# Optimization experiments

Hardware: AMD Instinct MI355X
Metric: run time of the kernel (lower is better)

Reference implementation:

```python
import jax, jax.numpy as jnp
import numpy as np

H = W = 240

def setup_inputs() -> dict:
    key = jax.random.key(0)
    k1, k2, k3 = jax.random.split(key, 3)
    B = 256
    T2_Gen = jax.random.normal(k1, (B, 1, H, W), dtype=jnp.float32)
    underT2_K = jax.random.normal(k2, (B, 2, H, W), dtype=jnp.float32)
    # k-space sampling mask (soft in [0,1); original uses a fixed undersampling mask)
    A = jax.random.uniform(k3, (H, W), dtype=jnp.float32)
    return {"T2_Gen": T2_Gen, "underT2_K": underT2_K, "A": A}

def reference(T2_Gen, underT2_K, A):
    # x2: [B, H, W]
    x2 = T2_Gen.reshape(-1, H, W)
    # batched 2D FFT over the last two axes (replaces the per-slice numpy loop)
    x2_k = jnp.fft.fft2(x2)  # complex64
    # undersampled k-space as complex: real = channel 0, imag = channel 1
    y_k = underT2_K[:, 0, :, :] + 1j * underT2_K[:, 1, :, :]
    z_k = (1.0 - A) * x2_k + y_k
    z = jnp.abs(jnp.fft.ifft2(z_k))  # [B, H, W] real
    return z.reshape(-1, 1, H, W)
```

## Files before the change

kernel.cpp:

```cpp
#include <hip/hip_runtime.h>
#include <hip/hip_fp16.h>
#include <math.h>

#define HW 240
#define PITCH 241
#define IMG_PIX (HW*HW)
#define NB 15
#define TILE_ELEMS (240*16)

__device__ __forceinline__ float2 cmul(float2 a, float2 b){
    return make_float2(a.x*b.x - a.y*b.y, a.x*b.y + a.y*b.x);
}
__device__ __forceinline__ float2 cadd(float2 a, float2 b){
    return make_float2(a.x+b.x, a.y+b.y);
}
__device__ __forceinline__ float2 csub(float2 a, float2 b){
    return make_float2(a.x-b.x, a.y-b.y);
}
__device__ __forceinline__ __half2 f2h(float2 a){ return __floats2half2_rn(a.x, a.y); }
__device__ __forceinline__ float2 h2f(__half2 h){ return make_float2(__low2float(h), __high2float(h)); }

template<int SIGN>
__device__ __forceinline__ void dft15(const float2* x, float2* X){
    const float S = (float)SIGN;
    const float s3 = 0.8660254037844387f;
    float2 y[5][3];
    #pragma unroll
    for (int n2 = 0; n2 < 5; ++n2){
        float2 a0 = x[n2], a1 = x[5+n2], a2 = x[10+n2];
        float2 t = cadd(a1, a2);
        float2 u = csub(a1, a2);
        float2 m = make_float2(a0.x - 0.5f*t.x, a0.y - 0.5f*t.y);
        float sx = S * s3;
        float2 s = make_float2(-sx*u.y, sx*u.x);
        y[n2][0] = cadd(a0, t);
        y[n2][1] = cadd(m, s);
        y[n2][2] = csub(m, s);
    }
    const float C15[9] = {1.f, 0.9135454576426009f, 0.6691306063588582f, 0.30901699437494745f,
                          -0.10452846326765346f, -0.5f, -0.8090169943749475f,
                          -0.9781476007338057f, -0.9781476007338057f};
    const float S15[9] = {0.f, 0.4067366430758004f, 0.7431448254773942f, 0.9510565162951535f,
                          0.9945218953682733f, 0.8660254037844387f, 0.5877852522924731f,
                          0.20791169081775931f, -0.20791169081775931f};
    #pragma unroll
    for (int n2 = 1; n2 < 5; ++n2){
        #pragma unroll
        for (int k1 = 1; k1 < 3; ++k1){
            const int e = n2*k1;
            y[n2][k1] = cmul(y[n2][k1], make_float2(C15[e], S*S15[e]));
        }
    }
    const float c1 = 0.30901699437494745f, s1 = 0.9510565162951535f;
    const float c2 = -0.8090169943749475f, s2 = 0.5877852522924731f;
    #pragma unroll
    for (int k1 = 0; k1 < 3; ++k1){
        float2 x0 = y[0][k1], x1 = y[1][k1], x2 = y[2][k1], x3 = y[3][k1], x4 = y[4][k1];
        float2 t1 = cadd(x1, x4), t3 = csub(x1, x4);
        float2 t2 = cadd(x2, x3), t4 = csub(x2, x3);
        X[k1] = make_float2(x0.x + t1.x + t2.x, x0.y + t1.y + t2.y);
        float2 u1 = make_float2(x0.x + c1*t1.x + c2*t2.x, x0.y + c1*t1.y + c2*t2.y);
        float2 u2 = make_float2(x0.x + c2*t1.x + c1*t2.x, x0.y + c2*t1.y + c1*t2.y);
        float2 v1 = make_float2(S*(s1*t3.x + s2*t4.x), S*(s1*t3.y + s2*t4.y));
        float2 v2 = make_float2(S*(s2*t3.x - s1*t4.x), S*(s2*t3.y - s1*t4.y));
        X[k1+3]  = make_float2(u1.x - v1.y, u1.y + v1.x);
        X[k1+12] = make_float2(u1.x + v1.y, u1.y - v1.x);
        X[k1+6]  = make_float2(u2.x - v2.y, u2.y + v2.x);
        X[k1+9]  = make_float2(u2.x + v2.y, u2.y - v2.x);
    }
}

template<int SIGN>
__device__ __forceinline__ void dft16(const float2* x, float2* X){
    const float S = (float)SIGN;
    float2 y[4][4];
    #pragma unroll
    for (int n2 = 0; n2 < 4; ++n2){
        float2 a0 = x[n2], a1 = x[4+n2], a2 = x[8+n2], a3 = x[12+n2];
        float2 t0 = cadd(a0,a2), t1 = csub(a0,a2);
        float2 t2 = cadd(a1,a3), t3 = csub(a1,a3);
        float2 it3 = make_float2(-S*t3.y, S*t3.x);
        y[n2][0] = cadd(t0,t2);
        y[n2][2] = csub(t0,t2);
        y[n2][1] = cadd(t1,it3);
        y[n2][3] = csub(t1,it3);
    }
    const float C16[10] = {1.f, 0.9238795325112867f, 0.7071067811865476f, 0.3826834323650898f,
                           0.f, -0.3826834323650898f, -0.7071067811865476f, -0.9238795325112867f,
                           -1.f, -0.9238795325112867f};
    const float S16[10] = {0.f, 0.3826834323650898f, 0.7071067811865476f, 0.9238795325112867f,
                           1.f, 0.9238795325112867f, 0.7071067811865476f, 0.3826834323650898f,
                           0.f, -0.3826834323650898f};
    #pragma unroll
    for (int n2 = 1; n2 < 4; ++n2){
        #pragma unroll
        for (int k1 = 1; k1 < 4; ++k1){
            const int e = n2*k1;
            y[n2][k1] = cmul(y[n2][k1], make_float2(C16[e], S*S16[e]));
        }
    }
    #pragma unroll
    for (int k1 = 0; k1 < 4; ++k1){
        float2 a0 = y[0][k1], a1 = y[1][k1], a2 = y[2][k1], a3 = y[3][k1];
        float2 t0 = cadd(a0,a2), t1 = csub(a0,a2);
        float2 t2 = cadd(a1,a3), t3 = csub(a1,a3);
        float2 it3 = make_float2(-S*t3.y, S*t3.x);
        X[k1]    = cadd(t0,t2);
        X[k1+8]  = csub(t0,t2);
        X[k1+4]  = cadd(t1,it3);
        X[k1+12] = csub(t1,it3);
    }
}

template<int SIGN>
__device__ void fft240(float2 (*sm)[PITCH], float2* v, int rl, int b){
    const float TWOPI = 6.28318530717958647692f;
    float2 Y[15];
    dft15<SIGN>(v, Y);
    float2 step, tw = make_float2(1.0f, 0.0f);
    {
        float ang = (float)SIGN * TWOPI * (float)b * (1.0f/240.0f);
        __sincosf(ang, &step.y, &step.x);
    }
    #pragma unroll
    for (int d = 0; d < 15; ++d){
        sm[rl][b*15 + d] = cmul(Y[d], tw);
        tw = cmul(tw, step);
    }
    __syncthreads();

    float2 Z[16];
    if (b < 15){
        #pragma unroll
        for (int bb = 0; bb < 16; ++bb) Z[bb] = sm[rl][bb*15 + b];
    }
    __syncthreads();
    if (b < 15){
        float2 XX[16];
        dft16<SIGN>(Z, XX);
        #pragma unroll
        for (int m = 0; m < 16; ++m) sm[rl][15*m + b] = XX[m];
    }
    __syncthreads();
}

__global__ __launch_bounds__(256) void passA_rowfft(const float* __restrict__ x,
                                                    __half2* __restrict__ out){
    __shared__ float2 sm[16][PITCH];
    float* smf = (float*)sm;
    int g = blockIdx.x, img = g / NB, h0 = (g % NB) * 16;
    int tid = threadIdx.x, rl = tid >> 4, b = tid & 15;
    const float* src = x + (size_t)img * IMG_PIX + (size_t)h0 * HW;
    #pragma unroll
    for (int j = 0; j < 15; ++j){
        int f = j*256 + tid;
        smf[(f/HW)*(2*PITCH) + (f%HW)] = src[f];
    }
    __syncthreads();
    float2 v[15];
    #pragma unroll
    for (int a = 0; a < 15; ++a) v[a] = make_float2(smf[rl*(2*PITCH) + 16*a + b], 0.0f);
    __syncthreads();
    fft240<-1>(sm, v, rl, b);
    int hl = rl, kwin = b;
    #pragma unroll
    for (int kb = 0; kb < NB; ++kb){
        float2 val = sm[hl][kb*16 + kwin];
        out[((size_t)(img*NB + kb)*HW + h0 + hl)*16 + kwin] = f2h(val);
    }
}

__global__ __launch_bounds__(256) void passB_col_dc_icol(const __half2* __restrict__ in,
                                                         const float* __restrict__ under,
                                                         const float* __restrict__ Am,
                                                         __half2* __restrict__ out){
    __shared__ float2 sm[16][PITCH];
    int g = blockIdx.x, img = g / NB, s = g % NB, kw0 = s * 16;
    int tid = threadIdx.x, rl = tid >> 4, b = tid & 15;
    const __half2* src = in + (size_t)(img*NB + s) * TILE_ELEMS;
    #pragma unroll
    for (int j = 0; j < 15; ++j){
        int f = j*256 + tid;
        sm[f & 15][f >> 4] = h2f(src[f]);
    }
    __syncthreads();
    float2 v[15];
    #pragma unroll
    for (int a = 0; a < 15; ++a) v[a] = sm[rl][16*a + b];
    __syncthreads();
    fft240<-1>(sm, v, rl, b);

    const float* y0 = under + (size_t)img * (2*IMG_PIX);
    const float* y1 = y0 + IMG_PIX;
    #pragma unroll
    for (int j = 0; j < 15; ++j){
        int kh = j*16 + rl;
        size_t p = (size_t)kh * HW + kw0 + b;
        float sc = 1.0f - Am[p];
        float2 X = sm[b][kh];
        sm[b][kh] = make_float2(sc * X.x + y0[p], sc * X.y + y1[p]);
    }
    __syncthreads();
    #pragma unroll
    for (int a = 0; a < 15; ++a) v[a] = sm[rl][16*a + b];
    __syncthreads();
    fft240<+1>(sm, v, rl, b);

    const float inv240 = 1.0f / 240.0f;
    __half2* dst = out + (size_t)(img*NB + s) * TILE_ELEMS;
    #pragma unroll
    for (int j = 0; j < 15; ++j){
        int f = j*256 + tid;
        float2 val = sm[f & 15][f >> 4];
        val.x *= inv240; val.y *= inv240;
        dst[f] = f2h(val);
    }
}

__global__ __launch_bounds__(256) void passC_irow_abs(const __half2* __restrict__ in,
                                                      float* __restrict__ outp){
    __shared__ float2 sm[16][PITCH];
    int g = blockIdx.x, img = g / NB, h0 = (g % NB) * 16;
    int tid = threadIdx.x, rl = tid >> 4, b = tid & 15;
    int hl = rl, kwin = b;
    #pragma unroll
    for (int kb = 0; kb < NB; ++kb){
        __half2 hv = in[((size_t)(img*NB + kb)*HW + h0 + hl)*16 + kwin];
        sm[hl][kb*16 + kwin] = h2f(hv);
    }
    __syncthreads();
    float2 v[15];
    #pragma unroll
    for (int a = 0; a < 15; ++a) v[a] = sm[rl][16*a + b];
    __syncthreads();
    fft240<+1>(sm, v, rl, b);
    float* dst = outp + (size_t)img * IMG_PIX + (size_t)h0 * HW;
    const float inv240 = 1.0f / 240.0f;
    #pragma unroll
    for (int j = 0; j < 15; ++j){
        int f = j*256 + tid;
        float2 X = sm[f/HW][f%HW];
        dst[f] = sqrtf(X.x*X.x + X.y*X.y) * inv240;
    }
}

extern "C" void kernel_launch(void* const* d_in, const int* in_sizes, int n_in,
                              void* d_out, int out_size, void* d_ws, size_t ws_size,
                              hipStream_t stream){
    const float* T2   = (const float*)d_in[0];
    const float* U    = (const float*)d_in[1];
    const float* Am   = (const float*)d_in[2];
    float* out        = (float*)d_out;

    const int B = 256;
    __half2* i1 = (__half2*)d_ws;
    __half2* i2 = i1 + (size_t)B * IMG_PIX;

    dim3 grid(B * NB), block(256);
    passA_rowfft     <<<grid, block, 0, stream>>>(T2, i1);
    passB_col_dc_icol<<<grid, block, 0, stream>>>(i1, U, Am, i2);
    passC_irow_abs   <<<grid, block, 0, stream>>>(i2, out);
}
```

Before: 283.6 us.

## Replace block-wide barriers with wave-local barriers in row FFT stages

Each wavefront of 64 lanes now owns four full rows of the 16-row tile, so the 240-point FFT only exchanges data within a single wave. This lets the block-wide __syncthreads calls inside the FFT and around the row loads and stores become wave barriers. Block barriers are kept only around the column transpose and the data-consistency step in passB. The aim is to remove the stall cost of block synchronisation, but correctness now depends on lockstep wave execution and on wave_barrier ordering LDS accesses.

```diff
diff --git a/kernel.cpp b/kernel.cpp
--- a/kernel.cpp
+++ b/kernel.cpp
@@ -113,7 +113,7 @@
 }
 
 template<int SIGN>
-__device__ void fft240(float2 (*sm)[PITCH], float2* v, int rl, int b){
+__device__ __forceinline__ void fft240_wave(float2 (*sm)[PITCH], float2* v, int row, int b){
     const float TWOPI = 6.28318530717958647692f;
     float2 Y[15];
     dft15<SIGN>(v, Y);
@@ -124,24 +124,20 @@
     }
     #pragma unroll
     for (int d = 0; d < 15; ++d){
-        sm[rl][b*15 + d] = cmul(Y[d], tw);
+        sm[row][b*15 + d] = cmul(Y[d], tw);
         tw = cmul(tw, step);
     }
-    __syncthreads();
-
-    float2 Z[16];
+    __builtin_amdgcn_wave_barrier();
     if (b < 15){
-        #pragma unroll
-        for (int bb = 0; bb < 16; ++bb) Z[bb] = sm[rl][bb*15 + b];
-    }
-    __syncthreads();
-    if (b < 15){
+        float2 Z[16];
+        #pragma unroll
+        for (int bb = 0; bb < 16; ++bb) Z[bb] = sm[row][bb*15 + b];
         float2 XX[16];
         dft16<SIGN>(Z, XX);
         #pragma unroll
-        for (int m = 0; m < 16; ++m) sm[rl][15*m + b] = XX[m];
-    }
-    __syncthreads();
+        for (int m = 0; m < 16; ++m) sm[row][15*m + b] = XX[m];
+    }
+    __builtin_amdgcn_wave_barrier();
 }
 
 __global__ __launch_bounds__(256) void passA_rowfft(const float* __restrict__ x,
@@ -149,24 +145,24 @@
     __shared__ float2 sm[16][PITCH];
     float* smf = (float*)sm;
     int g = blockIdx.x, img = g / NB, h0 = (g % NB) * 16;
-    int tid = threadIdx.x, rl = tid >> 4, b = tid & 15;
-    const float* src = x + (size_t)img * IMG_PIX + (size_t)h0 * HW;
-    #pragma unroll
-    for (int j = 0; j < 15; ++j){
-        int f = j*256 + tid;
-        smf[(f/HW)*(2*PITCH) + (f%HW)] = src[f];
-    }
-    __syncthreads();
+    int tid = threadIdx.x, wave = tid >> 6, lane = tid & 63;
+    int rl4 = lane >> 4, b = lane & 15, row = wave*4 + rl4;
+    const float* src = x + (size_t)img * IMG_PIX + (size_t)(h0 + wave*4) * HW;
+    #pragma unroll
+    for (int i = 0; i < 15; ++i){
+        int f = i*64 + lane;
+        smf[(wave*4 + f/HW)*(2*PITCH) + (f%HW)] = src[f];
+    }
+    __builtin_amdgcn_wave_barrier();
     float2 v[15];
     #pragma unroll
-    for (int a = 0; a < 15; ++a) v[a] = make_float2(smf[rl*(2*PITCH) + 16*a + b], 0.0f);
-    __syncthreads();
-    fft240<-1>(sm, v, rl, b);
-    int hl = rl, kwin = b;
+    for (int a = 0; a < 15; ++a) v[a] = make_float2(smf[row*(2*PITCH) + 16*a + b], 0.0f);
+    __builtin_amdgcn_wave_barrier();
+    fft240_wave<-1>(sm, v, row, b);
     #pragma unroll
     for (int kb = 0; kb < NB; ++kb){
-        float2 val = sm[hl][kb*16 + kwin];
-        out[((size_t)(img*NB + kb)*HW + h0 + hl)*16 + kwin] = f2h(val);
+        float2 val = sm[row][kb*16 + b];
+        out[((size_t)(img*NB + kb)*HW + h0 + wave*4 + rl4)*16 + b] = f2h(val);
     }
 }
 
@@ -176,41 +172,45 @@
                                                          __half2* __restrict__ out){
     __shared__ float2 sm[16][PITCH];
     int g = blockIdx.x, img = g / NB, s = g % NB, kw0 = s * 16;
-    int tid = threadIdx.x, rl = tid >> 4, b = tid & 15;
+    int tid = threadIdx.x, wave = tid >> 6, lane = tid & 63;
+    int rl4 = lane >> 4, b = lane & 15, row = wave*4 + rl4;
     const __half2* src = in + (size_t)(img*NB + s) * TILE_ELEMS;
     #pragma unroll
-    for (int j = 0; j < 15; ++j){
-        int f = j*256 + tid;
+    for (int i = 0; i < 15; ++i){
+        int f = i*256 + tid;
         sm[f & 15][f >> 4] = h2f(src[f]);
     }
     __syncthreads();
     float2 v[15];
     #pragma unroll
-    for (int a = 0; a < 15; ++a) v[a] = sm[rl][16*a + b];
-    __syncthreads();
-    fft240<-1>(sm, v, rl, b);
-
+    for (int a = 0; a < 15; ++a) v[a] = sm[row][16*a + b];
+    __builtin_amdgcn_wave_barrier();
+    fft240_wave<-1>(sm, v, row, b);
+    __syncthreads();
+
+    int rl = tid >> 4, bb = tid & 15;
     const float* y0 = under + (size_t)img * (2*IMG_PIX);
     const float* y1 = y0 + IMG_PIX;
     #pragma unroll
     for (int j = 0; j < 15; ++j){
         int kh = j*16 + rl;
-        size_t p = (size_t)kh * HW + kw0 + b;
+        size_t p = (size_t)kh * HW + kw0 + bb;
         float sc = 1.0f - Am[p];
-        float2 X = sm[b][kh];
-        sm[b][kh] = make_float2(sc * X.x + y0[p], sc * X.y + y1[p]);
-    }
-    __syncthreads();
-    #pragma unroll
-    for (int a = 0; a < 15; ++a) v[a] = sm[rl][16*a + b];
-    __syncthreads();
-    fft240<+1>(sm, v, rl, b);
+        float2 X = sm[bb][kh];
+        sm[bb][kh] = make_float2(sc * X.x + y0[p], sc * X.y + y1[p]);
+    }
+    __syncthreads();
+    #pragma unroll
+    for (int a = 0; a < 15; ++a) v[a] = sm[row][16*a + b];
+    __builtin_amdgcn_wave_barrier();
+    fft240_wave<+1>(sm, v, row, b);
+    __syncthreads();
 
     const float inv240 = 1.0f / 240.0f;
     __half2* dst = out + (size_t)(img*NB + s) * TILE_ELEMS;
     #pragma unroll
-    for (int j = 0; j < 15; ++j){
-        int f = j*256 + tid;
+    for (int i = 0; i < 15; ++i){
+        int f = i*256 + tid;
         float2 val = sm[f & 15][f >> 4];
         val.x *= inv240; val.y *= inv240;
         dst[f] = f2h(val);
@@ -221,25 +221,25 @@
                                                       float* __restrict__ outp){
     __shared__ float2 sm[16][PITCH];
     int g = blockIdx.x, img = g / NB, h0 = (g % NB) * 16;
-    int tid = threadIdx.x, rl = tid >> 4, b = tid & 15;
-    int hl = rl, kwin = b;
+    int tid = threadIdx.x, wave = tid >> 6, lane = tid & 63;
+    int rl4 = lane >> 4, b = lane & 15, row = wave*4 + rl4;
     #pragma unroll
     for (int kb = 0; kb < NB; ++kb){
-        __half2 hv = in[((size_t)(img*NB + kb)*HW + h0 + hl)*16 + kwin];
-        sm[hl][kb*16 + kwin] = h2f(hv);
-    }
-    __syncthreads();
+        __half2 hv = in[((size_t)(img*NB + kb)*HW + h0 + wave*4 + rl4)*16 + b];
+        sm[row][kb*16 + b] = h2f(hv);
+    }
+    __builtin_amdgcn_wave_barrier();
     float2 v[15];
     #pragma unroll
-    for (int a = 0; a < 15; ++a) v[a] = sm[rl][16*a + b];
-    __syncthreads();
-    fft240<+1>(sm, v, rl, b);
-    float* dst = outp + (size_t)img * IMG_PIX + (size_t)h0 * HW;
+    for (int a = 0; a < 15; ++a) v[a] = sm[row][16*a + b];
+    __builtin_amdgcn_wave_barrier();
+    fft240_wave<+1>(sm, v, row, b);
+    float* dst = outp + (size_t)img * IMG_PIX + (size_t)(h0 + wave*4) * HW;
     const float inv240 = 1.0f / 240.0f;
     #pragma unroll
-    for (int j = 0; j < 15; ++j){
-        int f = j*256 + tid;
-        float2 X = sm[f/HW][f%HW];
+    for (int i = 0; i < 15; ++i){
+        int f = i*64 + lane;
+        float2 X = sm[wave*4 + f/HW][f%HW];
         dst[f] = sqrtf(X.x*X.x + X.y*X.y) * inv240;
     }
 }
```

Measured after the change: 284.8 us. About the same (+0.4%).
